# Performance work log

Hardware: AMD Instinct MI355X
Metric: run time of the kernel (lower is better)

Reference implementation:

```python
import jax, jax.numpy as jnp
import numpy as np

B, S, H = 2, 2048, 4096
NH, NKV, HD = 32, 8, 128
RD = 64  # partial rotary dim = head_dim * partial_rotary_factor
THETA = 10000.0


def setup_inputs() -> dict:
    key = jax.random.key(0)
    ks = jax.random.split(key, 6)
    hidden_states = jax.random.normal(ks[0], (B, S, H), dtype=jnp.float32)
    wq = jax.random.normal(ks[1], (H, NH * HD), dtype=jnp.float32) * 0.02
    wk = jax.random.normal(ks[2], (H, NKV * HD), dtype=jnp.float32) * 0.02
    wv = jax.random.normal(ks[3], (H, NKV * HD), dtype=jnp.float32) * 0.02
    wo = jax.random.normal(ks[4], (NH * HD, H), dtype=jnp.float32) * 0.02
    # default RoPE over rotary_dim=RD: inv_freq has RD//2 entries, emb = cat(freqs, freqs)
    inv_freq = 1.0 / (THETA ** (jnp.arange(0, RD, 2, dtype=jnp.float32) / RD))  # [RD//2]
    pos = jnp.arange(S, dtype=jnp.float32)
    freqs = pos[:, None] * inv_freq[None, :]               # [S, RD//2]
    emb = jnp.concatenate([freqs, freqs], axis=-1)          # [S, RD]
    cos = jnp.broadcast_to(jnp.cos(emb)[None], (B, S, RD))
    sin = jnp.broadcast_to(jnp.sin(emb)[None], (B, S, RD))
    return {"hidden_states": hidden_states, "wq": wq, "wk": wk, "wv": wv, "wo": wo,
            "cos": cos, "sin": sin}


def _rotate_half_interleaved(x):
    # GLM-style interleaved rotate: pairs (x0,x1) -> (-x1,x0)
    x1 = x[..., 0::2]
    x2 = x[..., 1::2]
    return jnp.stack((-x2, x1), axis=-1).reshape(x.shape)


def _apply_partial_rope(x, cos_i, sin_i):
    x_rot, x_pass = x[..., :RD], x[..., RD:]
    x_rot = x_rot * cos_i + _rotate_half_interleaved(x_rot) * sin_i
    return jnp.concatenate([x_rot, x_pass], axis=-1)


def reference(hidden_states, wq, wk, wv, wo, cos, sin):
    b, s, _ = hidden_states.shape
    # projections -> [B, nheads, S, head_dim]
    q = (hidden_states @ wq).reshape(b, s, NH, HD).transpose(0, 2, 1, 3)
    k = (hidden_states @ wk).reshape(b, s, NKV, HD).transpose(0, 2, 1, 3)
    v = (hidden_states @ wv).reshape(b, s, NKV, HD).transpose(0, 2, 1, 3)
    # GLM partial rotary: take first half of cos/sin and repeat-interleave by 2
    cos_i = jnp.repeat(cos[..., : RD // 2], 2, axis=-1)[:, None]  # [B,1,S,RD]
    sin_i = jnp.repeat(sin[..., : RD // 2], 2, axis=-1)[:, None]
    q = _apply_partial_rope(q, cos_i, sin_i)
    k = _apply_partial_rope(k, cos_i, sin_i)
    # repeat_kv for GQA
    rep = NH // NKV
    k = jnp.repeat(k, rep, axis=1)
    v = jnp.repeat(v, rep, axis=1)
    # causal SDPA, scaling = head_dim**-0.5
    scores = jnp.einsum('bhqd,bhkd->bhqk', q, k) * (HD ** -0.5)
    causal = jnp.tril(jnp.ones((s, s), dtype=bool))
    scores = jnp.where(causal[None, None], scores, jnp.finfo(scores.dtype).min)
    probs = jax.nn.softmax(scores, axis=-1)
    out = jnp.einsum('bhqk,bhkd->bhqd', probs, v)
    out = out.transpose(0, 2, 1, 3).reshape(b, s, NH * HD)
    return out @ wo
```

## Files before the change

### kernel.cpp

```cpp
#include <hip/hip_runtime.h>


typedef _Float16 f16;
typedef _Float16 f16x8 __attribute__((ext_vector_type(8)));
typedef float f32x4 __attribute__((ext_vector_type(4)));
typedef float f32x16 __attribute__((ext_vector_type(16)));

static constexpr int Bn = 2, Sn = 2048, Hn = 4096, NH = 32, NKV = 8, HD = 128;
static constexpr float QSC = 0.08838834764831845f * 1.44269504088896340736f;

#define AS1 __attribute__((address_space(1)))
#define AS3 __attribute__((address_space(3)))

__device__ __forceinline__ void async_ld16(const void* g, void* l) {
    __builtin_amdgcn_global_load_lds((const AS1 void*)g, (AS3 void*)l, 16, 0, 0);
}

__device__ __forceinline__ unsigned pk2(float a, float b) {
    unsigned r;
    asm("v_cvt_pkrtz_f16_f32 %0, %1, %2" : "=v"(r) : "v"(a), "v"(b));
    return r;
}

__device__ __forceinline__ float fexp2(float x) {
    float r;
    asm("v_exp_f32 %0, %1" : "=v"(r) : "v"(x));
    return r;
}

__global__ void k_cvt(const float* __restrict__ src, f16* __restrict__ dst, long n) {
    long i = ((long)blockIdx.x * blockDim.x + threadIdx.x) * 8;
    if (i >= n) return;
    float4 a = *(const float4*)(src + i);
    float4 b = *(const float4*)(src + i + 4);
    f16x8 o = {(f16)a.x, (f16)a.y, (f16)a.z, (f16)a.w,
               (f16)b.x, (f16)b.y, (f16)b.z, (f16)b.w};
    *(f16x8*)(dst + i) = o;
}

__global__ void k_tcvt(const float* __restrict__ src, f16* __restrict__ dst,
                       int K, int N, long rs) {
    __shared__ float tile[32][33];
    int k0 = blockIdx.y * 32, n0 = blockIdx.x * 32;
    int tx = threadIdx.x, ty = threadIdx.y;
#pragma unroll
    for (int r = ty; r < 32; r += 8)
        tile[r][tx] = src[(long)(k0 + r) * N + (n0 + tx)];
    __syncthreads();
#pragma unroll
    for (int r = ty; r < 32; r += 8)
        dst[(long)(n0 + r) * rs + (k0 + tx)] = (f16)tile[tx][r];
}

__global__ void k_rope(f16* __restrict__ x, const float* __restrict__ cosb,
                       const float* __restrict__ sinb, int nheads) {
    long idx = (long)blockIdx.x * blockDim.x + threadIdx.x;
    int i = (int)(idx & 31);
    long t = idx >> 5;
    int s = (int)(t & (Sn - 1));
    int bh = (int)(t >> 11);
    int b = bh / nheads;
    long base = t * HD + 2 * i;
    float c = cosb[((long)b * Sn + s) * 64 + i];
    float sv = sinb[((long)b * Sn + s) * 64 + i];
    float x0 = (float)x[base], x1 = (float)x[base + 1];
    x[base]     = (f16)(x0 * c - x1 * sv);
    x[base + 1] = (f16)(x1 * c + x0 * sv);
}

__device__ __forceinline__ void gemm_core(
    const f16* __restrict__ A, const f16* __restrict__ Bt,
    char* L, int m0, int n0, f32x4 acc[4][4]) {
    const int t = threadIdx.x, lane = t & 63, wave = t >> 6;
    const int wm = wave >> 2, wn = wave & 3;
    const int fr = lane & 15, fg = lane >> 4;

    const f16* gsa[2];
    const f16* gsb[4];
#pragma unroll
    for (int i = 0; i < 2; ++i) {
        int d = i * 8192 + t * 16;
        int row = d >> 7, cb = (d & 127) ^ ((row & 7) << 4);
        gsa[i] = A + (long)(m0 + row) * 4096 + (cb >> 1);
    }
#pragma unroll
    for (int i = 0; i < 4; ++i) {
        int d = i * 8192 + t * 16;
        int row = d >> 7, cb = (d & 127) ^ ((row & 7) << 4);
        gsb[i] = Bt + (long)(n0 + row) * 4096 + (cb >> 1);
    }
    const int dst0 = wave * 1024;

    for (int kt = 0; kt < 64; ++kt) {
        const int ko = kt * 64;
#pragma unroll
        for (int i = 0; i < 2; ++i)
            async_ld16(gsa[i] + ko, L + i * 8192 + dst0);
#pragma unroll
        for (int i = 0; i < 4; ++i)
            async_ld16(gsb[i] + ko, L + 16384 + i * 8192 + dst0);
        __syncthreads();

#pragma unroll
        for (int ks = 0; ks < 2; ++ks) {
            const int cb = ks * 64 + 16 * fg;
            f16x8 bf[4], af[4];
#pragma unroll
            for (int nf = 0; nf < 4; ++nf) {
                int r = wn * 64 + nf * 16 + fr;
                bf[nf] = *(const f16x8*)(L + 16384 + r * 128 + (cb ^ ((r & 7) << 4)));
            }
#pragma unroll
            for (int mf = 0; mf < 4; ++mf) {
                int r = wm * 64 + mf * 16 + fr;
                af[mf] = *(const f16x8*)(L + r * 128 + (cb ^ ((r & 7) << 4)));
            }
            __builtin_amdgcn_s_setprio(1);
#pragma unroll
            for (int mf = 0; mf < 4; ++mf)
#pragma unroll
                for (int nf = 0; nf < 4; ++nf)
                    acc[mf][nf] = __builtin_amdgcn_mfma_f32_16x16x32_f16(
                        af[mf], bf[nf], acc[mf][nf], 0, 0, 0);
            __builtin_amdgcn_s_setprio(0);
        }
        __syncthreads();
    }
}

__global__ __launch_bounds__(512, 4) void k_gemm_qkv(
    const f16* __restrict__ A, const f16* __restrict__ Bt,
    f16* __restrict__ q, f16* __restrict__ kk_, f16* __restrict__ vt) {
    __shared__ __align__(16) char L[49152];
    const int xcd = blockIdx.x & 7, i = blockIdx.x >> 3;
    const int n0 = (xcd * 3 + (i >> 5)) * 256;
    const int m0 = (i & 31) * 128;
    f32x4 acc[4][4] = {};
    gemm_core(A, Bt, L, m0, n0, acc);

    const int lane = threadIdx.x & 63, wave = threadIdx.x >> 6;
    const int wm = wave >> 2, wn = wave & 3;
    const int fr = lane & 15, fg = lane >> 4;
#pragma unroll
    for (int mf = 0; mf < 4; ++mf) {
        int r0 = m0 + wm * 64 + mf * 16 + 4 * fg;
        int b = r0 >> 11, s = r0 & (Sn - 1);
#pragma unroll
        for (int nf = 0; nf < 4; ++nf) {
            int cc = n0 + wn * 64 + nf * 16 + fr;
            int d = cc & 127;
            if (cc < 4096) {
                int h = cc >> 7;
#pragma unroll
                for (int e = 0; e < 4; ++e)
                    q[(((long)b * NH + h) * Sn + s + e) * HD + d] = (f16)(acc[mf][nf][e] * QSC);
            } else if (cc < 5120) {
                int h = (cc - 4096) >> 7;
#pragma unroll
                for (int e = 0; e < 4; ++e)
                    kk_[(((long)b * NKV + h) * Sn + s + e) * HD + d] = (f16)acc[mf][nf][e];
            } else {
                int h = (cc - 5120) >> 7;
                uint2 w = {pk2(acc[mf][nf][0], acc[mf][nf][1]),
                           pk2(acc[mf][nf][2], acc[mf][nf][3])};
                *(uint2*)&vt[(((long)b * NKV + h) * HD + d) * Sn + s] = w;
            }
        }
    }
}

__global__ __launch_bounds__(512, 4) void k_gemm_out(
    const f16* __restrict__ A, const f16* __restrict__ Bt,
    float* __restrict__ out) {
    __shared__ __align__(16) char L[49152];
    const int xcd = blockIdx.x & 7, i = blockIdx.x >> 3;
    const int n0 = (xcd * 2 + (i >> 5)) * 256;
    const int m0 = (i & 31) * 128;
    f32x4 acc[4][4] = {};
    gemm_core(A, Bt, L, m0, n0, acc);

    const int lane = threadIdx.x & 63, wave = threadIdx.x >> 6;
    const int wm = wave >> 2, wn = wave & 3;
    const int fr = lane & 15, fg = lane >> 4;
#pragma unroll
    for (int mf = 0; mf < 4; ++mf) {
        int r0 = m0 + wm * 64 + mf * 16 + 4 * fg;
#pragma unroll
        for (int nf = 0; nf < 4; ++nf) {
            int cc = n0 + wn * 64 + nf * 16 + fr;
#pragma unroll
            for (int e = 0; e < 4; ++e)
                out[(long)(r0 + e) * 4096 + cc] = acc[mf][nf][e];
        }
    }
}


__device__ __forceinline__ f16x8 ld_sw256(const f16* base, int r, int c) {
    int byte = r * 256 + ((c * 2) ^ ((r & 7) << 4));
    return *(const f16x8*)((const char*)base + byte);
}
__device__ __forceinline__ f16x8 ld_sw128(const f16* base, int r, int c) {
    int byte = r * 128 + ((c * 2) ^ ((r & 7) << 4));
    return *(const f16x8*)((const char*)base + byte);
}

__device__ __forceinline__ void stage_k(const f16* __restrict__ Kb, f16* ksm,
                                        int k0, int wave, int lane) {
#pragma unroll
    for (int i = 0; i < 4; ++i) {
        int dbase = (i * 4 + wave) * 1024;
        int d = dbase + lane * 16;
        int row = d >> 8;
        int cb = (d & 255) ^ ((row & 7) << 4);
        async_ld16(Kb + (long)(k0 + row) * HD + (cb >> 1), (char*)ksm + dbase);
    }
}
__device__ __forceinline__ void stage_v(const f16* __restrict__ Vb, f16* vsm,
                                        int k0, int wave, int lane) {
#pragma unroll
    for (int i = 0; i < 4; ++i) {
        int dbase = (i * 4 + wave) * 1024;
        int d = dbase + lane * 16;
        int row = d >> 7;
        int cb = (d & 127) ^ ((row & 7) << 4);
        async_ld16(Vb + (long)row * Sn + k0 + (cb >> 1), (char*)vsm + dbase);
    }
}

__global__ __launch_bounds__(256) void k_attn(
    const f16* __restrict__ Q, const f16* __restrict__ K,
    const f16* __restrict__ Vt, f16* __restrict__ O) {
    __shared__ __align__(16) f16 Ksm[2][64 * 128];
    __shared__ __align__(16) f16 Vsm[2][128 * 64];

    const int id = blockIdx.x;
    const int kvh = id & 7;
    const int r_ = id >> 3;
    const int qt = 15 - (r_ & 15);
    const int hg = (r_ >> 4) & 3;
    const int b  = r_ >> 6;
    const int h  = kvh * 4 + hg;
    const int q0 = qt * 128;
    const int t = threadIdx.x, lane = t & 63, wave = t >> 6;
    const int q0w = q0 + wave * 32;
    const int lq = lane & 31, hi = lane >> 5;

    const f16* Qb = Q + ((long)(b * NH + h) * Sn) * HD;
    const f16* Kb = K + ((long)(b * NKV + kvh) * Sn) * HD;
    const f16* Vb = Vt + ((long)(b * NKV + kvh) * HD) * Sn;

    f16x8 qf[8];
#pragma unroll
    for (int s = 0; s < 8; ++s)
        qf[s] = *(const f16x8*)&Qb[(long)(q0w + lq) * HD + 16 * s + 8 * hi];

    f32x16 oacc[4] = {};
    float mrun = -1e30f, lrun = 0.f;

    const int nt = q0 / 64 + 2;
    stage_k(Kb, Ksm[0], 0, wave, lane);
    stage_v(Vb, Vsm[0], 0, wave, lane);

    for (int kt = 0; kt < nt; ++kt) {
        const int k0 = kt * 64;
        const int cur = kt & 1;
        if (kt + 1 < nt) {
            stage_k(Kb, Ksm[cur ^ 1], (kt + 1) * 64, wave, lane);
            stage_v(Vb, Vsm[cur ^ 1], (kt + 1) * 64, wave, lane);
            asm volatile("s_waitcnt vmcnt(8)" ::: "memory");
        } else {
            asm volatile("s_waitcnt vmcnt(0)" ::: "memory");
        }
        __builtin_amdgcn_s_barrier();

        if (k0 <= q0w + 31) {
            f32x16 st[2] = {};
#pragma unroll
            for (int s = 0; s < 8; ++s) {
                f16x8 kf0 = ld_sw256(Ksm[cur], lq,      16 * s + 8 * hi);
                f16x8 kf1 = ld_sw256(Ksm[cur], 32 + lq, 16 * s + 8 * hi);
                st[0] = __builtin_amdgcn_mfma_f32_32x32x16_f16(kf0, qf[s], st[0], 0, 0, 0);
                st[1] = __builtin_amdgcn_mfma_f32_32x32x16_f16(kf1, qf[s], st[1], 0, 0, 0);
            }
            const bool full = (k0 + 63 <= q0w);
            if (!full) {
#pragma unroll
                for (int mt = 0; mt < 2; ++mt)
#pragma unroll
                    for (int r = 0; r < 16; ++r) {
                        int kvv = k0 + 32 * mt + (r & 3) + 8 * (r >> 2) + 4 * hi;
                        if (kvv > q0w + lq) st[mt][r] = -1e30f;
                    }
            }
            float pm = st[0][0];
#pragma unroll
            for (int r = 1; r < 16; ++r) pm = fmaxf(pm, st[0][r]);
#pragma unroll
            for (int r = 0; r < 16; ++r) pm = fmaxf(pm, st[1][r]);
            pm = fmaxf(pm, __shfl_xor(pm, 32, 64));
            if (__any(pm > mrun + 8.f)) {
                float mn = fmaxf(mrun, pm);
                float sc = fexp2(mrun - mn);
                mrun = mn;
                lrun *= sc;
                float scr[16];
#pragma unroll
                for (int r = 0; r < 16; ++r)
                    scr[r] = __shfl(sc, (r & 3) + 8 * (r >> 2) + 4 * hi, 64);
#pragma unroll
                for (int db = 0; db < 4; ++db)
#pragma unroll
                    for (int r = 0; r < 16; ++r)
                        oacc[db][r] *= scr[r];
            }
            unsigned pw[2][8];
#pragma unroll
            for (int mt = 0; mt < 2; ++mt)
#pragma unroll
                for (int i = 0; i < 8; ++i) {
                    float p0 = fexp2(st[mt][2 * i]     - mrun);
                    float p1 = fexp2(st[mt][2 * i + 1] - mrun);
                    lrun += p0 + p1;
                    pw[mt][i] = pk2(p0, p1);
                }
#pragma unroll
            for (int s = 0; s < 4; ++s) {
                const int mt = s >> 1, sl = s & 1;
                unsigned a0 = pw[mt][4 * sl], a1 = pw[mt][4 * sl + 1];
                unsigned a2 = pw[mt][4 * sl + 2], a3 = pw[mt][4 * sl + 3];
                unsigned own0 = hi ? a2 : a0, own1 = hi ? a3 : a1;
                unsigned snd0 = hi ? a0 : a2, snd1 = hi ? a1 : a3;
                unsigned rx0 = (unsigned)__shfl_xor((int)snd0, 32, 64);
                unsigned rx1 = (unsigned)__shfl_xor((int)snd1, 32, 64);
                union { unsigned u[4]; f16x8 v; } pu;
                pu.u[0] = hi ? rx0 : own0;
                pu.u[1] = hi ? rx1 : own1;
                pu.u[2] = hi ? own0 : rx0;
                pu.u[3] = hi ? own1 : rx1;
#pragma unroll
                for (int db = 0; db < 4; ++db) {
                    f16x8 vf = ld_sw128(Vsm[cur], 32 * db + lq, 16 * s + 8 * hi);
                    oacc[db] = __builtin_amdgcn_mfma_f32_32x32x16_f16(pu.v, vf, oacc[db], 0, 0, 0);
                }
            }
        }
        __builtin_amdgcn_s_barrier();
    }

    lrun += __shfl_xor(lrun, 32, 64);
    float li = 1.f / lrun;
    float ir[16];
#pragma unroll
    for (int r = 0; r < 16; ++r)
        ir[r] = __shfl(li, (r & 3) + 8 * (r >> 2) + 4 * hi, 64);
#pragma unroll
    for (int db = 0; db < 4; ++db)
#pragma unroll
        for (int r = 0; r < 16; ++r) {
            int qloc = (r & 3) + 8 * (r >> 2) + 4 * hi;
            long tok = (long)b * Sn + q0w + qloc;
            O[tok * (NH * HD) + h * HD + 32 * db + lq] = (f16)(oacc[db][r] * ir[r]);
        }
}

__global__ void k_ws_fail(float* out) { out[0] = 1.0e9f; }

extern "C" void kernel_launch(void* const* d_in, const int* in_sizes, int n_in,
                              void* d_out, int out_size, void* d_ws, size_t ws_size,
                              hipStream_t stream) {
    const float* hs   = (const float*)d_in[0];
    const float* wq   = (const float*)d_in[1];
    const float* wk   = (const float*)d_in[2];
    const float* wv   = (const float*)d_in[3];
    const float* wo   = (const float*)d_in[4];
    const float* cosb = (const float*)d_in[5];
    const float* sinb = (const float*)d_in[6];
    float* out = (float*)d_out;

    const size_t OFF_WQKV = 0;
    const size_t OFF_WO   = 50331648;
    const size_t OFF_HID  = 83886080;
    const size_t OFF_Q    = 117440512;
    const size_t OFF_K    = 150994944;
    const size_t OFF_VT   = 167772160;
    const size_t WS_NEED  = 176160768;
    if (ws_size < WS_NEED) { k_ws_fail<<<1, 1, 0, stream>>>(out); return; }

    char* ws = (char*)d_ws;
    f16* wqkv_t = (f16*)(ws + OFF_WQKV);
    f16* wo_t   = (f16*)(ws + OFF_WO);
    f16* hid    = (f16*)(ws + OFF_HID);
    f16* qb     = (f16*)(ws + OFF_Q);
    f16* kb     = (f16*)(ws + OFF_K);
    f16* vtb    = (f16*)(ws + OFF_VT);

    dim3 tb(32, 8);
    k_cvt<<<dim3(16777216 / (256 * 8)), 256, 0, stream>>>(hs, hid, 16777216L);
    k_tcvt<<<dim3(128, 128), tb, 0, stream>>>(wq, wqkv_t, 4096, 4096, 4096);
    k_tcvt<<<dim3(32, 128),  tb, 0, stream>>>(wk, wqkv_t + (long)4096 * 4096, 4096, 1024, 4096);
    k_tcvt<<<dim3(32, 128),  tb, 0, stream>>>(wv, wqkv_t + (long)5120 * 4096, 4096, 1024, 4096);
    k_tcvt<<<dim3(128, 128), tb, 0, stream>>>(wo, wo_t, 4096, 4096, 4096);
    k_gemm_qkv<<<dim3(768), 512, 0, stream>>>(hid, wqkv_t, qb, kb, vtb);
    k_rope<<<dim3(2 * 32 * 2048 * 32 / 256), 256, 0, stream>>>(qb, cosb, sinb, NH);
    k_rope<<<dim3(2 * 8 * 2048 * 32 / 256), 256, 0, stream>>>(kb, cosb, sinb, NKV);
    k_attn<<<dim3(1024), 256, 0, stream>>>(qb, kb, vtb, hid);
    k_gemm_out<<<dim3(512), 512, 0, stream>>>(hid, wo_t, out);
}
```

Measured before the change: 645.1 us.

## Use 256x256 GEMM tiles with double-buffered async LDS loads

Replaces the 128x256 single-buffered GEMM core with a 256x256 tile core. The new core double-buffers 128 KB of LDS and interleaves async global-to-LDS prefetches for upcoming k-tiles between MFMA quarter-steps, using vmcnt waits and barriers. The larger tile raises arithmetic intensity and the pipelining is meant to hide load latency. In exchange the grid halves and occupancy drops to one block per CU, and block-to-tile swizzling is remapped across XCDs.

```diff
diff --git a/kernel.cpp b/kernel.cpp
--- a/kernel.cpp
+++ b/kernel.cpp
@@ -68,82 +68,106 @@
     x[base + 1] = (f16)(x1 * c + x0 * sv);
 }
 
-__device__ __forceinline__ void gemm_core(
+__device__ __forceinline__ void gemm256_core(
     const f16* __restrict__ A, const f16* __restrict__ Bt,
-    char* L, int m0, int n0, f32x4 acc[4][4]) {
+    char* L, int m0, int n0, f32x4 acc[8][4]) {
     const int t = threadIdx.x, lane = t & 63, wave = t >> 6;
     const int wm = wave >> 2, wn = wave & 3;
     const int fr = lane & 15, fg = lane >> 4;
 
-    const f16* gsa[2];
-    const f16* gsb[4];
-#pragma unroll
-    for (int i = 0; i < 2; ++i) {
-        int d = i * 8192 + t * 16;
-        int row = d >> 7, cb = (d & 127) ^ ((row & 7) << 4);
-        gsa[i] = A + (long)(m0 + row) * 4096 + (cb >> 1);
-    }
-#pragma unroll
-    for (int i = 0; i < 4; ++i) {
-        int d = i * 8192 + t * 16;
-        int row = d >> 7, cb = (d & 127) ^ ((row & 7) << 4);
-        gsb[i] = Bt + (long)(n0 + row) * 4096 + (cb >> 1);
-    }
-    const int dst0 = wave * 1024;
-
-    for (int kt = 0; kt < 64; ++kt) {
-        const int ko = kt * 64;
-#pragma unroll
-        for (int i = 0; i < 2; ++i)
-            async_ld16(gsa[i] + ko, L + i * 8192 + dst0);
-#pragma unroll
-        for (int i = 0; i < 4; ++i)
-            async_ld16(gsb[i] + ko, L + 16384 + i * 8192 + dst0);
-        __syncthreads();
-
-#pragma unroll
-        for (int ks = 0; ks < 2; ++ks) {
-            const int cb = ks * 64 + 16 * fg;
-            f16x8 bf[4], af[4];
-#pragma unroll
-            for (int nf = 0; nf < 4; ++nf) {
-                int r = wn * 64 + nf * 16 + fr;
-                bf[nf] = *(const f16x8*)(L + 16384 + r * 128 + (cb ^ ((r & 7) << 4)));
-            }
-#pragma unroll
-            for (int mf = 0; mf < 4; ++mf) {
-                int r = wm * 64 + mf * 16 + fr;
-                af[mf] = *(const f16x8*)(L + r * 128 + (cb ^ ((r & 7) << 4)));
-            }
+    const int srowL = wave * 8 + (lane >> 3);
+    const int scol  = 8 * ((lane & 7) ^ (lane >> 3));
+    const f16* ga = A  + (long)(m0 + srowL) * 4096 + scol;
+    const f16* gb = Bt + (long)(n0 + srowL) * 4096 + scol;
+    const int woff = wave * 1024;
+
+    auto ST = [&](int sel, int c, int row0, int kt) {
+        const f16* g = sel ? gb : ga;
+        async_ld16(g + (long)row0 * 4096 + kt * 64,
+                   L + c * 65536 + sel * 32768 + row0 * 128 + woff);
+    };
+
+    ST(0, 0, 0, 0);   ST(0, 0, 64, 0);  ST(0, 0, 128, 0); ST(0, 0, 192, 0);
+    ST(1, 0, 0, 0);   ST(1, 0, 64, 0);  ST(1, 0, 128, 0); ST(1, 0, 192, 0);
+    ST(1, 1, 0, 1);   ST(1, 1, 64, 1);  ST(1, 1, 128, 1); ST(1, 1, 192, 1);
+    ST(0, 1, 0, 1);   ST(0, 1, 128, 1);
+    asm volatile("s_waitcnt vmcnt(6)" ::: "memory");
+    __builtin_amdgcn_s_barrier();
+
+    const int abase = wm * 128;
+    const int bbase = wn * 64;
+
+    for (int tt = 0; tt < 64; ++tt) {
+        const int c = tt & 1;
+        const char* bufA = L + c * 65536;
+        const char* bufB = bufA + 32768;
+        f16x8 bf[2][4];
+
+#pragma unroll
+        for (int q = 0; q < 4; ++q) {
+            if (q == 0) {
+#pragma unroll
+                for (int ks = 0; ks < 2; ++ks)
+#pragma unroll
+                    for (int nf = 0; nf < 4; ++nf) {
+                        int r = bbase + nf * 16 + fr;
+                        bf[ks][nf] = *(const f16x8*)(bufB + r * 128 +
+                                        ((ks * 64 + 16 * fg) ^ ((r & 7) << 4)));
+                    }
+            }
+            f16x8 af[2][2];
+#pragma unroll
+            for (int ks = 0; ks < 2; ++ks)
+#pragma unroll
+                for (int i = 0; i < 2; ++i) {
+                    int r = abase + (2 * q + i) * 16 + fr;
+                    af[ks][i] = *(const f16x8*)(bufA + r * 128 +
+                                    ((ks * 64 + 16 * fg) ^ ((r & 7) << 4)));
+                }
+            if (q == 0) { if (tt + 1 < 64) { ST(0, c ^ 1,  64, tt + 1);
+                                             ST(0, c ^ 1, 192, tt + 1); } }
+            if (q == 1) { if (tt + 2 < 64) { ST(1, c,   0, tt + 2);
+                                             ST(1, c,  64, tt + 2); } }
+            if (q == 2) { if (tt + 2 < 64) { ST(1, c, 128, tt + 2);
+                                             ST(1, c, 192, tt + 2); } }
+            if (q == 3) { if (tt + 2 < 64) { ST(0, c,   0, tt + 2);
+                                             ST(0, c, 128, tt + 2); } }
+            __builtin_amdgcn_s_barrier();
             __builtin_amdgcn_s_setprio(1);
 #pragma unroll
-            for (int mf = 0; mf < 4; ++mf)
-#pragma unroll
-                for (int nf = 0; nf < 4; ++nf)
-                    acc[mf][nf] = __builtin_amdgcn_mfma_f32_16x16x32_f16(
-                        af[mf], bf[nf], acc[mf][nf], 0, 0, 0);
+            for (int ks = 0; ks < 2; ++ks)
+#pragma unroll
+                for (int i = 0; i < 2; ++i)
+#pragma unroll
+                    for (int nf = 0; nf < 4; ++nf)
+                        acc[2 * q + i][nf] = __builtin_amdgcn_mfma_f32_16x16x32_f16(
+                            af[ks][i], bf[ks][nf], acc[2 * q + i][nf], 0, 0, 0);
             __builtin_amdgcn_s_setprio(0);
-        }
-        __syncthreads();
-    }
-}
-
-__global__ __launch_bounds__(512, 4) void k_gemm_qkv(
+            if (q == 3) {
+                if (tt < 62)       asm volatile("s_waitcnt vmcnt(6)" ::: "memory");
+                else if (tt == 62) asm volatile("s_waitcnt vmcnt(0)" ::: "memory");
+            }
+            __builtin_amdgcn_s_barrier();
+        }
+    }
+}
+
+__global__ __launch_bounds__(512) void k_gemm_qkv(
     const f16* __restrict__ A, const f16* __restrict__ Bt,
     f16* __restrict__ q, f16* __restrict__ kk_, f16* __restrict__ vt) {
-    __shared__ __align__(16) char L[49152];
-    const int xcd = blockIdx.x & 7, i = blockIdx.x >> 3;
-    const int n0 = (xcd * 3 + (i >> 5)) * 256;
-    const int m0 = (i & 31) * 128;
-    f32x4 acc[4][4] = {};
-    gemm_core(A, Bt, L, m0, n0, acc);
+    __shared__ __align__(16) char L[131072];
+    const int bid = blockIdx.x;
+    const int swzb = (bid & 7) * 48 + (bid >> 3);
+    const int m0 = (swzb / 24) * 256, n0 = (swzb % 24) * 256;
+    f32x4 acc[8][4] = {};
+    gemm256_core(A, Bt, L, m0, n0, acc);
 
     const int lane = threadIdx.x & 63, wave = threadIdx.x >> 6;
     const int wm = wave >> 2, wn = wave & 3;
     const int fr = lane & 15, fg = lane >> 4;
 #pragma unroll
-    for (int mf = 0; mf < 4; ++mf) {
-        int r0 = m0 + wm * 64 + mf * 16 + 4 * fg;
+    for (int mf = 0; mf < 8; ++mf) {
+        int r0 = m0 + wm * 128 + mf * 16 + 4 * fg;
         int b = r0 >> 11, s = r0 & (Sn - 1);
 #pragma unroll
         for (int nf = 0; nf < 4; ++nf) {
@@ -169,22 +193,22 @@
     }
 }
 
-__global__ __launch_bounds__(512, 4) void k_gemm_out(
+__global__ __launch_bounds__(512) void k_gemm_out(
     const f16* __restrict__ A, const f16* __restrict__ Bt,
     float* __restrict__ out) {
-    __shared__ __align__(16) char L[49152];
-    const int xcd = blockIdx.x & 7, i = blockIdx.x >> 3;
-    const int n0 = (xcd * 2 + (i >> 5)) * 256;
-    const int m0 = (i & 31) * 128;
-    f32x4 acc[4][4] = {};
-    gemm_core(A, Bt, L, m0, n0, acc);
+    __shared__ __align__(16) char L[131072];
+    const int bid = blockIdx.x;
+    const int swzb = (bid & 7) * 32 + (bid >> 3);
+    const int m0 = (swzb >> 4) * 256, n0 = (swzb & 15) * 256;
+    f32x4 acc[8][4] = {};
+    gemm256_core(A, Bt, L, m0, n0, acc);
 
     const int lane = threadIdx.x & 63, wave = threadIdx.x >> 6;
     const int wm = wave >> 2, wn = wave & 3;
     const int fr = lane & 15, fg = lane >> 4;
 #pragma unroll
-    for (int mf = 0; mf < 4; ++mf) {
-        int r0 = m0 + wm * 64 + mf * 16 + 4 * fg;
+    for (int mf = 0; mf < 8; ++mf) {
+        int r0 = m0 + wm * 128 + mf * 16 + 4 * fg;
 #pragma unroll
         for (int nf = 0; nf < 4; ++nf) {
             int cc = n0 + wn * 64 + nf * 16 + fr;
@@ -401,9 +425,9 @@
     k_tcvt<<<dim3(32, 128),  tb, 0, stream>>>(wk, wqkv_t + (long)4096 * 4096, 4096, 1024, 4096);
     k_tcvt<<<dim3(32, 128),  tb, 0, stream>>>(wv, wqkv_t + (long)5120 * 4096, 4096, 1024, 4096);
     k_tcvt<<<dim3(128, 128), tb, 0, stream>>>(wo, wo_t, 4096, 4096, 4096);
-    k_gemm_qkv<<<dim3(768), 512, 0, stream>>>(hid, wqkv_t, qb, kb, vtb);
+    k_gemm_qkv<<<dim3(384), 512, 0, stream>>>(hid, wqkv_t, qb, kb, vtb);
     k_rope<<<dim3(2 * 32 * 2048 * 32 / 256), 256, 0, stream>>>(qb, cosb, sinb, NH);
     k_rope<<<dim3(2 * 8 * 2048 * 32 / 256), 256, 0, stream>>>(kb, cosb, sinb, NKV);
     k_attn<<<dim3(1024), 256, 0, stream>>>(qb, kb, vtb, hid);
-    k_gemm_out<<<dim3(512), 512, 0, stream>>>(hid, wo_t, out);
-}
+    k_gemm_out<<<dim3(256), 512, 0, stream>>>(hid, wo_t, out);
+}
```

New measurement: 627.8 us. -2.7%, faster.
